# Optimization experiments

Measured on AMD Instinct MI355X. Metric: run time of the kernel, lower is better.

## Reference

```python
import jax, jax.numpy as jnp
import numpy as np

L, I, H = 4, 256, 512          # layers, input_size, hidden_size
SH, LH, GH = 4, 2, 2            # short/long/global heads
NH, HD, FF = SH + LH + GH, H // (SH + LH + GH), 2 * H
S, B = 1024, 8                  # seq (AST nodes), batch
EPS = 1e-5
NEG = -1e9


def _ln(x, g, b):
    m = jnp.mean(x, axis=-1, keepdims=True)
    v = jnp.var(x, axis=-1, keepdims=True)
    return (x - m) * jax.lax.rsqrt(v + EPS) * g + b


def setup_inputs() -> dict:
    key = jax.random.key(0)
    ks = jax.random.split(key, 10)
    w = lambda k, shape: jax.random.normal(k, shape, jnp.float32) * 0.02
    return {
        "nodes": jax.random.normal(ks[0], (S, B, I), jnp.float32),
        "dist": jax.random.randint(ks[1], (B, S, S), 0, 5, jnp.int32),
        "dense_w": w(ks[2], (H, I)), "dense_b": jnp.zeros((H,), jnp.float32),
        "dense_ln_g": jnp.ones((H,), jnp.float32), "dense_ln_b": jnp.zeros((H,), jnp.float32),
        "qkv_w": w(ks[3], (L, 3 * H, H)), "qkv_b": jnp.zeros((L, 3 * H), jnp.float32),
        "out_w": w(ks[4], (L, H, H)), "out_b": jnp.zeros((L, H), jnp.float32),
        "ln1_g": jnp.ones((L, H), jnp.float32), "ln1_b": jnp.zeros((L, H), jnp.float32),
        "ffn_w1": w(ks[5], (L, FF, H)), "ffn_b1": jnp.zeros((L, FF), jnp.float32),
        "ffn_w2": w(ks[6], (L, H, FF)), "ffn_b2": jnp.zeros((L, H), jnp.float32),
        "ln2_g": jnp.ones((L, H), jnp.float32), "ln2_b": jnp.zeros((L, H), jnp.float32),
        "bn_g": jnp.ones((H,), jnp.float32), "bn_b": jnp.zeros((H,), jnp.float32),
    }


def _mask_bias(dist):
    # dist: [B,S,S] int -> additive bias [B,NH,S,S]
    short = (dist == 1)[:, None]                       # [B,1,S,S]
    longm = (dist >= 1)[:, None]
    globm = jnp.broadcast_to((dist[:, 0:1, :] >= 1)[:, None], (dist.shape[0], 1, S, S))
    allowed = jnp.concatenate([
        jnp.broadcast_to(short, (dist.shape[0], SH, S, S)),
        jnp.broadcast_to(longm, (dist.shape[0], LH, S, S)),
        jnp.broadcast_to(globm, (dist.shape[0], GH, S, S)),
    ], axis=1)
    allowed = allowed | jnp.eye(S, dtype=bool)
    return jnp.where(allowed, 0.0, NEG).astype(jnp.float32)


def _forward(nodes, dist, dense_w, dense_b, dense_ln_g, dense_ln_b,
             qkv_w, qkv_b, out_w, out_b, ln1_g, ln1_b,
             ffn_w1, ffn_b1, ffn_w2, ffn_b2, ln2_g, ln2_b, bn_g, bn_b):
    x = jnp.transpose(nodes, (1, 0, 2))                # [B,S,I]
    x = _ln(x @ dense_w.T + dense_b, dense_ln_g, dense_ln_b)  # [B,S,H]
    bias = _mask_bias(dist)                            # [B,NH,S,S]
    scale = 1.0 / np.sqrt(HD)

    def layer(x, p):
        (wqkv, bqkv, wo, bo, g1, b1, w1, bf1, w2, bf2, g2, b2) = p
        qkv = x @ wqkv.T + bqkv                        # [B,S,3H]
        q, k, v = jnp.split(qkv, 3, axis=-1)
        q = q.reshape(B, S, NH, HD).transpose(0, 2, 1, 3)
        k = k.reshape(B, S, NH, HD).transpose(0, 2, 1, 3)
        v = v.reshape(B, S, NH, HD).transpose(0, 2, 1, 3)
        scores = jnp.einsum('bhqd,bhkd->bhqk', q, k) * scale + bias
        attn = jax.nn.softmax(scores, axis=-1)
        o = jnp.einsum('bhqk,bhkd->bhqd', attn, v)
        o = o.transpose(0, 2, 1, 3).reshape(B, S, H) @ wo.T + bo
        x = _ln(x + o, g1, b1)
        f = jax.nn.relu(x @ w1.T + bf1) @ w2.T + bf2
        x = _ln(x + f, g2, b2)
        return x, None

    params = (qkv_w, qkv_b, out_w, out_b, ln1_g, ln1_b,
              ffn_w1, ffn_b1, ffn_w2, ffn_b2, ln2_g, ln2_b)
    x, _ = jax.lax.scan(layer, x, params)
    hidden = x[:, 0]                                   # first token -> [B,H]
    m = jnp.mean(hidden, axis=0)
    v = jnp.var(hidden, axis=0)
    return (hidden - m) * jax.lax.rsqrt(v + EPS) * bn_g + bn_b


def reference(nodes, dist, dense_w, dense_b, dense_ln_g, dense_ln_b,
              qkv_w, qkv_b, out_w, out_b, ln1_g, ln1_b,
              ffn_w1, ffn_b1, ffn_w2, ffn_b2, ln2_g, ln2_b, bn_g, bn_b):
    return _forward(nodes, dist, dense_w, dense_b, dense_ln_g, dense_ln_b,
                    qkv_w, qkv_b, out_w, out_b, ln1_g, ln1_b,
                    ffn_w1, ffn_b1, ffn_w2, ffn_b2, ln2_g, ln2_b, bn_g, bn_b)
```

## Files before the change

kernel.cpp:

```cpp
#include <hip/hip_runtime.h>
#include <hip/hip_bf16.h>
#include <math.h>

#define LAYERS 4
#define IDIM 256
#define HDIM 512
#define NH 8
#define HD 64
#define FF 1024
#define SEQ 1024
#define BATCH 8
#define EPS 1e-5f

typedef __attribute__((ext_vector_type(8))) short short8;
typedef __attribute__((ext_vector_type(4))) short short4v;
typedef __attribute__((ext_vector_type(4))) float f32x4;
typedef __attribute__((ext_vector_type(4))) int int4v;
typedef __attribute__((ext_vector_type(4))) unsigned int uint4v;
typedef unsigned long long u64;

__device__ __forceinline__ short f2bf(float f) {
    unsigned u = __float_as_uint(f);
    u = (u + 0x7FFFu + ((u >> 16) & 1u)) >> 16;
    return (short)u;
}
__device__ __forceinline__ float bf2f(short s) {
    return __uint_as_float(((unsigned)(unsigned short)s) << 16);
}
__device__ __forceinline__ void gll16(const void* g, void* l) {
    __builtin_amdgcn_global_load_lds(
        (const __attribute__((address_space(1))) unsigned int*)g,
        (__attribute__((address_space(3))) unsigned int*)l, 16, 0, 0);
}
__device__ __forceinline__ float fexp2(float x) {
#if __has_builtin(__builtin_amdgcn_exp2f)
    return __builtin_amdgcn_exp2f(x);
#else
    return exp2f(x);
#endif
}

#define CVT_P0 131072u
#define CVT_P1 3276800u
#define CVT_P2 4325376u
#define CVT_P3 6422528u
#define CVT_TOT 8519680u
#define PREP_W 8320
#define PREP_N 2048
__global__ __launch_bounds__(256) void prep_all(
    const float* __restrict__ s0, short* __restrict__ d0,
    const float* __restrict__ s1, short* __restrict__ d1,
    const float* __restrict__ s2, short* __restrict__ d2,
    const float* __restrict__ s3, short* __restrict__ d3,
    const float* __restrict__ s4, short* __restrict__ d4,
    const float* __restrict__ nodes, short* __restrict__ xt,
    const int* __restrict__ dist, u64* __restrict__ mS,
    u64* __restrict__ mL, u64* __restrict__ mG) {
    int blk = blockIdx.x;
    if (blk < PREP_W) {
        size_t i = ((size_t)blk * 256 + threadIdx.x) * 4;
        const float* s; short* d; size_t off;
        if (i < CVT_P0)      { s = s0; d = d0; off = i; }
        else if (i < CVT_P1) { s = s1; d = d1; off = i - CVT_P0; }
        else if (i < CVT_P2) { s = s2; d = d2; off = i - CVT_P1; }
        else if (i < CVT_P3) { s = s3; d = d3; off = i - CVT_P2; }
        else                 { s = s4; d = d4; off = i - CVT_P3; }
        f32x4 f = *(const f32x4*)(s + off);
        short4v o = {f2bf(f[0]), f2bf(f[1]), f2bf(f[2]), f2bf(f[3])};
        *(short4v*)(d + off) = o;
    } else if (blk < PREP_W + PREP_N) {
        size_t idx = ((size_t)(blk - PREP_W) * 256 + threadIdx.x) * 4;
        int i  = idx & (IDIM - 1);
        int sb = idx >> 8;
        int b  = sb & (BATCH - 1);
        int s  = sb >> 3;
        f32x4 f = *(const f32x4*)(nodes + idx);
        short4v o = {f2bf(f[0]), f2bf(f[1]), f2bf(f[2]), f2bf(f[3])};
        *(short4v*)(xt + ((size_t)b * SEQ + s) * IDIM + i) = o;
    } else {
        int blk2 = blk - (PREP_W + PREP_N);
        int b = blk2 >> 10, q = blk2 & 1023;
        int wv = threadIdx.x >> 6, lane = threadIdx.x & 63;
        const int* dp = dist + ((size_t)b * SEQ + q) * SEQ;
        size_t mbase = ((size_t)b * SEQ + q) * 16;
#pragma unroll
        for (int it = 0; it < 4; it++) {
            int w64 = it * 4 + wv;
            int d = dp[w64 * 64 + lane];
            u64 bs = __ballot(d == 1);
            u64 bl = __ballot(d >= 1);
            if (lane == 0) {
                mS[mbase + w64] = bs;
                mL[mbase + w64] = bl;
                if (q == 0) mG[b * 16 + w64] = bl;
            }
        }
    }
}

template<int BM, int BK>
__global__ __launch_bounds__(256, 2)
void gemm_bf16(const short* __restrict__ A, const short* __restrict__ W,
               const float* __restrict__ bias, short* __restrict__ C,
               short* __restrict__ vt, int M, int N, int K, int relu) {
    constexpr int UPR = BK / 8;
    constexpr int RPC = 512 / BK;
    __shared__ __align__(16) short As[BM * BK];
    __shared__ __align__(16) short Ws[128 * BK];
    const int tid = threadIdx.x;
    const int w = tid >> 6, lane = tid & 63;
    const int l15 = lane & 15, quad = lane >> 4;
    const int m0 = blockIdx.y * BM, n0 = blockIdx.x * 128;

    constexpr int NI = (BM == 128) ? 4 : 2;
    const int wm = (BM == 128) ? (w >> 1) * 64 : 0;
    const int wn = (BM == 128) ? (w & 1) * 64 : w * 32;

    f32x4 acc[4][NI];
#pragma unroll
    for (int mi = 0; mi < 4; mi++)
#pragma unroll
        for (int ni = 0; ni < NI; ni++) acc[mi][ni] = (f32x4){0.f, 0.f, 0.f, 0.f};

    const int r_in = (BK == 64) ? (lane >> 3) : (lane >> 4);
    const int c8   = lane & (UPR - 1);

    for (int k0 = 0; k0 < K; k0 += BK) {
#pragma unroll
        for (int rep = 0; rep < BM * BK / 2048; rep++) {
            int chunk = rep * 4 + w;
            int row = chunk * RPC + r_in;
            const short* src = A + (size_t)(m0 + row) * K + k0 + ((c8 ^ (row & (UPR - 1))) << 3);
            gll16(src, (char*)As + chunk * 1024);
        }
#pragma unroll
        for (int rep = 0; rep < 128 * BK / 2048; rep++) {
            int chunk = rep * 4 + w;
            int row = chunk * RPC + r_in;
            const short* src = W + (size_t)(n0 + row) * K + k0 + ((c8 ^ (row & (UPR - 1))) << 3);
            gll16(src, (char*)Ws + chunk * 1024);
        }
        __syncthreads();
#pragma unroll
        for (int ks = 0; ks < BK / 32; ks++) {
            short8 af[4], wf[NI];
            const int dblk = ks * 4 + quad;
#pragma unroll
            for (int mi = 0; mi < 4; mi++) {
                int row = wm + mi * 16 + l15;
                af[mi] = *(const short8*)((const char*)As + row * (BK * 2) + ((dblk ^ (row & (UPR - 1))) << 4));
            }
#pragma unroll
            for (int ni = 0; ni < NI; ni++) {
                int row = wn + ni * 16 + l15;
                wf[ni] = *(const short8*)((const char*)Ws + row * (BK * 2) + ((dblk ^ (row & (UPR - 1))) << 4));
            }
#pragma unroll
            for (int mi = 0; mi < 4; mi++)
#pragma unroll
                for (int ni = 0; ni < NI; ni++)
                    acc[mi][ni] = __builtin_amdgcn_mfma_f32_16x16x32_bf16(
                        af[mi], wf[ni], acc[mi][ni], 0, 0, 0);
        }
        __syncthreads();
    }
    if (vt && n0 >= 1024) {
#pragma unroll
        for (int ni = 0; ni < NI; ni++) {
            int n = n0 + wn + ni * 16 + l15;
            int d = n - 1024, h = d >> 6, dd = d & 63;
            float bz = bias[n];
#pragma unroll
            for (int mi = 0; mi < 4; mi++) {
                int mbase = m0 + wm + mi * 16 + quad * 4;
                int b = mbase >> 10, s = mbase & 1023;
                size_t off = ((size_t)(b * NH + h) * HD + dd) * SEQ + s;
                short4v pk;
#pragma unroll
                for (int r = 0; r < 4; r++) pk[r] = f2bf(acc[mi][ni][r] + bz);
                *(short4v*)(vt + off) = pk;
            }
        }
    } else {
#pragma unroll
        for (int ni = 0; ni < NI; ni++) {
            int n = n0 + wn + ni * 16 + l15;
            float bz = bias[n];
#pragma unroll
            for (int mi = 0; mi < 4; mi++) {
#pragma unroll
                for (int r = 0; r < 4; r++) {
                    int m = m0 + wm + mi * 16 + quad * 4 + r;
                    float v = acc[mi][ni][r] + bz;
                    if (relu) v = fmaxf(v, 0.f);
                    C[(size_t)m * N + n] = f2bf(v);
                }
            }
        }
    }
}

template<int K, bool RES>
__global__ __launch_bounds__(512, 1)
void gemm_ln(const short* __restrict__ A, const short* __restrict__ W,
             const float* __restrict__ bias, const short* __restrict__ resid,
             const float* __restrict__ g, const float* __restrict__ bta,
             short* __restrict__ Y) {
    constexpr int BK = 64, BM = 32, NW = 512, NT = K / BK;
    __shared__ __align__(16) short As[2][BM * BK];
    __shared__ __align__(16) short Ws[2][NW * BK];
    const int tid = threadIdx.x, w = tid >> 6, lane = tid & 63;
    const int l15 = lane & 15, quad = lane >> 4;
    const int m0 = blockIdx.x * BM;
    const int r_in = lane >> 3, c8 = lane & 7;
    const int swz = (c8 ^ r_in) << 3;

    f32x4 acc[2][4];
#pragma unroll
    for (int mi = 0; mi < 2; mi++)
#pragma unroll
        for (int ni = 0; ni < 4; ni++) acc[mi][ni] = (f32x4){0.f, 0.f, 0.f, 0.f};

#define STAGE_LN(bf, k0)                                                          \
    do {                                                                          \
        if (w < 4) {                                                              \
            int row_ = w * 8 + r_in;                                              \
            gll16(A + (size_t)(m0 + row_) * K + (k0) + swz,                       \
                  (char*)As[bf] + w * 1024);                                      \
        }                                                                         \
        _Pragma("unroll")                                                         \
        for (int rep_ = 0; rep_ < 8; rep_++) {                                    \
            int chunk_ = rep_ * 8 + w;                                            \
            int row_ = chunk_ * 8 + r_in;                                         \
            gll16(W + (size_t)row_ * K + (k0) + swz,                              \
                  (char*)Ws[bf] + chunk_ * 1024);                                 \
        }                                                                         \
    } while (0)

    STAGE_LN(0, 0);
    __syncthreads();
    int cur = 0;
    for (int t = 0; t < NT; t++) {
        if (t + 1 < NT) STAGE_LN(cur ^ 1, (t + 1) * BK);
#pragma unroll
        for (int ks = 0; ks < 2; ks++) {
            const int dblk = ks * 4 + quad;
            short8 af[2];
#pragma unroll
            for (int mi = 0; mi < 2; mi++) {
                int row = mi * 16 + l15;
                af[mi] = *(const short8*)((const char*)As[cur] + row * 128 + ((dblk ^ (row & 7)) << 4));
            }
#pragma unroll
            for (int ni = 0; ni < 4; ni++) {
                int row = w * 64 + ni * 16 + l15;
                short8 wf = *(const short8*)((const char*)Ws[cur] + row * 128 + ((dblk ^ (row & 7)) << 4));
#pragma unroll
                for (int mi = 0; mi < 2; mi++)
                    acc[mi][ni] = __builtin_amdgcn_mfma_f32_16x16x32_bf16(
                        wf, af[mi], acc[mi][ni], 0, 0, 0);
            }
        }
        __syncthreads();
        cur ^= 1;
    }
#undef STAGE_LN

    float sum[2] = {0.f, 0.f}, sq[2] = {0.f, 0.f};
#pragma unroll
    for (int mi = 0; mi < 2; mi++)
#pragma unroll
        for (int ni = 0; ni < 4; ni++) {
            int nb = w * 64 + ni * 16 + quad * 4;
            f32x4 bz = *(const f32x4*)(bias + nb);
            f32x4 v;
            if (RES) {
                short4v rv = *(const short4v*)(resid + (size_t)(m0 + mi * 16 + l15) * NW + nb);
#pragma unroll
                for (int r = 0; r < 4; r++) v[r] = acc[mi][ni][r] + bz[r] + bf2f(rv[r]);
            } else {
#pragma unroll
                for (int r = 0; r < 4; r++) v[r] = acc[mi][ni][r] + bz[r];
            }
            acc[mi][ni] = v;
            sum[mi] += v[0] + v[1] + v[2] + v[3];
            sq[mi]  += v[0] * v[0] + v[1] * v[1] + v[2] * v[2] + v[3] * v[3];
        }
#pragma unroll
    for (int mi = 0; mi < 2; mi++) {
        sum[mi] += __shfl_xor(sum[mi], 16); sum[mi] += __shfl_xor(sum[mi], 32);
        sq[mi]  += __shfl_xor(sq[mi], 16);  sq[mi]  += __shfl_xor(sq[mi], 32);
    }
    float* red = (float*)As;
    if (quad == 0) {
#pragma unroll
        for (int mi = 0; mi < 2; mi++) {
            red[(mi * 16 + l15) * 8 + w]       = sum[mi];
            red[256 + (mi * 16 + l15) * 8 + w] = sq[mi];
        }
    }
    __syncthreads();
    float mean[2], inv[2];
#pragma unroll
    for (int mi = 0; mi < 2; mi++) {
        f32x4 s0 = *(const f32x4*)(red + (mi * 16 + l15) * 8);
        f32x4 s1 = *(const f32x4*)(red + (mi * 16 + l15) * 8 + 4);
        f32x4 q0 = *(const f32x4*)(red + 256 + (mi * 16 + l15) * 8);
        f32x4 q1 = *(const f32x4*)(red + 256 + (mi * 16 + l15) * 8 + 4);
        float st = s0[0] + s0[1] + s0[2] + s0[3] + s1[0] + s1[1] + s1[2] + s1[3];
        float qt = q0[0] + q0[1] + q0[2] + q0[3] + q1[0] + q1[1] + q1[2] + q1[3];
        float mn = st * (1.f / NW);
        float vr = qt * (1.f / NW) - mn * mn;
        mean[mi] = mn;
        inv[mi]  = rsqrtf(vr + EPS);
    }
#pragma unroll
    for (int mi = 0; mi < 2; mi++)
#pragma unroll
        for (int ni = 0; ni < 4; ni++) {
            int nb = w * 64 + ni * 16 + quad * 4;
            f32x4 gv = *(const f32x4*)(g + nb);
            f32x4 bv = *(const f32x4*)(bta + nb);
            short4v pk;
#pragma unroll
            for (int r = 0; r < 4; r++)
                pk[r] = f2bf((acc[mi][ni][r] - mean[mi]) * inv[mi] * gv[r] + bv[r]);
            *(short4v*)(Y + (size_t)(m0 + mi * 16 + l15) * NW + nb) = pk;
        }
}

__global__ __launch_bounds__(512, 1)
void fused_ffn(const short* __restrict__ X, const short* __restrict__ W1,
               const float* __restrict__ b1, const short* __restrict__ W2,
               const float* __restrict__ b2, const float* __restrict__ g,
               const float* __restrict__ bta, short* __restrict__ Y) {
    __shared__ __align__(16) char smem[135168];
    short* As1 = (short*)smem;
    char*  W1s = smem + 4096;
    char*  Hs  = smem;
    char*  W2s = smem + 65536;
    float* red = (float*)(smem + 131072);

    const int tid = threadIdx.x, w = tid >> 6, lane = tid & 63;
    const int l15 = lane & 15, quad = lane >> 4;
    const int m0 = blockIdx.x * 32;
    const int r_in = lane >> 3, c8 = lane & 7;
    const int swz = (c8 ^ r_in) << 3;

    f32x4 acc1[2][8];
#pragma unroll
    for (int mi = 0; mi < 2; mi++)
#pragma unroll
        for (int ni = 0; ni < 8; ni++) acc1[mi][ni] = (f32x4){0.f, 0.f, 0.f, 0.f};

    for (int t = 0; t < 8; t++) {
        if (w < 4) {
            int row = w * 8 + r_in;
            gll16(X + (size_t)(m0 + row) * HDIM + t * 64 + swz,
                  (char*)As1 + w * 1024);
        }
#pragma unroll
        for (int rep = 0; rep < 16; rep++) {
            int c = rep * 8 + w;
            int row = c * 8 + r_in;
            gll16(W1 + (size_t)row * HDIM + t * 64 + swz, W1s + c * 1024);
        }
        __syncthreads();
#pragma unroll
        for (int ks = 0; ks < 2; ks++) {
            const int dblk = ks * 4 + quad;
            short8 af[2];
#pragma unroll
            for (int mi = 0; mi < 2; mi++) {
                int row = mi * 16 + l15;
                af[mi] = *(const short8*)((const char*)As1 + row * 128 + ((dblk ^ (row & 7)) << 4));
            }
#pragma unroll
            for (int ni = 0; ni < 8; ni++) {
                int row = w * 128 + ni * 16 + l15;
                short8 wf = *(const short8*)(W1s + row * 128 + ((dblk ^ (row & 7)) << 4));
#pragma unroll
                for (int mi = 0; mi < 2; mi++)
                    acc1[mi][ni] = __builtin_amdgcn_mfma_f32_16x16x32_bf16(
                        wf, af[mi], acc1[mi][ni], 0, 0, 0);
            }
        }
        __syncthreads();
    }

#pragma unroll
    for (int mi = 0; mi < 2; mi++)
#pragma unroll
        for (int ni = 0; ni < 8; ni++) {
            int n = w * 128 + ni * 16 + quad * 4;
            f32x4 bz = *(const f32x4*)(b1 + n);
            short4v pk;
#pragma unroll
            for (int r = 0; r < 4; r++)
                pk[r] = f2bf(fmaxf(acc1[mi][ni][r] + bz[r], 0.f));
            int row = mi * 16 + l15;
            int u = n >> 3;
            *(short4v*)(Hs + row * 2048 + ((u ^ (row & 7)) << 4) + (quad & 1) * 8) = pk;
        }

    f32x4 acc2[2][4];
#pragma unroll
    for (int mi = 0; mi < 2; mi++)
#pragma unroll
        for (int ni = 0; ni < 4; ni++) acc2[mi][ni] = (f32x4){0.f, 0.f, 0.f, 0.f};

    for (int t2 = 0; t2 < 16; t2++) {
#pragma unroll
        for (int rep = 0; rep < 8; rep++) {
            int c = rep * 8 + w;
            int row = c * 8 + r_in;
            gll16(W2 + (size_t)row * FF + t2 * 64 + swz, W2s + c * 1024);
        }
        __syncthreads();
#pragma unroll
        for (int ks = 0; ks < 2; ks++) {
            const int dblk = ks * 4 + quad;
            short8 af[2];
#pragma unroll
            for (int mi = 0; mi < 2; mi++) {
                int row = mi * 16 + l15;
                af[mi] = *(const short8*)(Hs + row * 2048 + (((t2 * 8 + dblk) ^ (row & 7)) << 4));
            }
#pragma unroll
            for (int ni = 0; ni < 4; ni++) {
                int row = w * 64 + ni * 16 + l15;
                short8 wf = *(const short8*)(W2s + row * 128 + ((dblk ^ (row & 7)) << 4));
#pragma unroll
                for (int mi = 0; mi < 2; mi++)
                    acc2[mi][ni] = __builtin_amdgcn_mfma_f32_16x16x32_bf16(
                        wf, af[mi], acc2[mi][ni], 0, 0, 0);
            }
        }
        __syncthreads();
    }

    float sum[2] = {0.f, 0.f}, sq[2] = {0.f, 0.f};
#pragma unroll
    for (int mi = 0; mi < 2; mi++)
#pragma unroll
        for (int ni = 0; ni < 4; ni++) {
            int nb = w * 64 + ni * 16 + quad * 4;
            f32x4 bz = *(const f32x4*)(b2 + nb);
            short4v rv = *(const short4v*)(X + (size_t)(m0 + mi * 16 + l15) * HDIM + nb);
            f32x4 v;
#pragma unroll
            for (int r = 0; r < 4; r++) v[r] = acc2[mi][ni][r] + bz[r] + bf2f(rv[r]);
            acc2[mi][ni] = v;
            sum[mi] += v[0] + v[1] + v[2] + v[3];
            sq[mi]  += v[0] * v[0] + v[1] * v[1] + v[2] * v[2] + v[3] * v[3];
        }
#pragma unroll
    for (int mi = 0; mi < 2; mi++) {
        sum[mi] += __shfl_xor(sum[mi], 16); sum[mi] += __shfl_xor(sum[mi], 32);
        sq[mi]  += __shfl_xor(sq[mi], 16);  sq[mi]  += __shfl_xor(sq[mi], 32);
    }
    if (quad == 0) {
#pragma unroll
        for (int mi = 0; mi < 2; mi++) {
            red[(mi * 16 + l15) * 8 + w]       = sum[mi];
            red[256 + (mi * 16 + l15) * 8 + w] = sq[mi];
        }
    }
    __syncthreads();
    float mean[2], inv[2];
#pragma unroll
    for (int mi = 0; mi < 2; mi++) {
        f32x4 s0 = *(const f32x4*)(red + (mi * 16 + l15) * 8);
        f32x4 s1 = *(const f32x4*)(red + (mi * 16 + l15) * 8 + 4);
        f32x4 q0 = *(const f32x4*)(red + 256 + (mi * 16 + l15) * 8);
        f32x4 q1 = *(const f32x4*)(red + 256 + (mi * 16 + l15) * 8 + 4);
        float st = s0[0] + s0[1] + s0[2] + s0[3] + s1[0] + s1[1] + s1[2] + s1[3];
        float qt = q0[0] + q0[1] + q0[2] + q0[3] + q1[0] + q1[1] + q1[2] + q1[3];
        float mn = st * (1.f / HDIM);
        float vr = qt * (1.f / HDIM) - mn * mn;
        mean[mi] = mn;
        inv[mi]  = rsqrtf(vr + EPS);
    }
#pragma unroll
    for (int mi = 0; mi < 2; mi++)
#pragma unroll
        for (int ni = 0; ni < 4; ni++) {
            int nb = w * 64 + ni * 16 + quad * 4;
            f32x4 gv = *(const f32x4*)(g + nb);
            f32x4 bv = *(const f32x4*)(bta + nb);
            short4v pk;
#pragma unroll
            for (int r = 0; r < 4; r++)
                pk[r] = f2bf((acc2[mi][ni][r] - mean[mi]) * inv[mi] * gv[r] + bv[r]);
            *(short4v*)(Y + (size_t)(m0 + mi * 16 + l15) * HDIM + nb) = pk;
        }
}

#define EXP2SC 0.18033688011112042f
__global__ __launch_bounds__(256, 4)
void attn_mfma(const short* __restrict__ qkv, const short* __restrict__ vt,
               const u64* __restrict__ maskS, const u64* __restrict__ maskL,
               const u64* __restrict__ maskG, short* __restrict__ out) {
    const int tid = threadIdx.x;
    const int w = tid >> 6, lane = tid & 63, l15 = lane & 15, quad = lane >> 4;
    const int p = blockIdx.x;
    const int g_ = (p & 7) + 8 * (p >> 7);
    const int qt = (p >> 3) & 15;
    const int b = g_ >> 3, h = g_ & 7;
    const int q = qt * 64 + w * 16 + l15;

    __shared__ __align__(16) short Ks[128 * 64];
    __shared__ __align__(16) short Vs[128 * 64];

    short8 qf[2];
    {
        const short* qrow = qkv + ((size_t)(b * SEQ + q) * 1536) + h * 64;
#pragma unroll
        for (int ks = 0; ks < 2; ks++)
            qf[ks] = *(const short8*)(qrow + ks * 32 + quad * 8);
    }
    const u64* mrow = (h < 4) ? (maskS + ((size_t)b * SEQ + q) * 16)
                   : (h < 6) ? (maskL + ((size_t)b * SEQ + q) * 16)
                   :           (maskG + (size_t)b * 16);

    f32x4 of[4];
#pragma unroll
    for (int mt = 0; mt < 4; mt++) of[mt] = (f32x4){0.f, 0.f, 0.f, 0.f};
    float ls0 = 0.f, ls1 = 0.f;

    const int r_in = lane >> 3, c8 = lane & 7;
    const int swz = (c8 ^ r_in) << 3;
    const short* kbase = qkv + ((size_t)b * SEQ) * 1536 + 512 + h * 64 + swz;
    const short* vp = vt + ((size_t)((b * NH + h) * HD) + r_in) * SEQ + swz;
    const int fsw = (l15 & 7);

    for (int kt = 0; kt < SEQ; kt += 128) {
#pragma unroll
        for (int rep = 0; rep < 4; rep++) {
            int c = rep * 4 + w;
            int pr = c * 8 + r_in;
            int pt = pr & 63;
            int key = (pr & 64) | (pt & 32) | (((pt >> 2) & 3) << 3)
                    | (((pt >> 4) & 1) << 2) | (pt & 3);
            gll16(kbase + (size_t)(kt + key) * 1536, (char*)Ks + c * 1024);
        }
#pragma unroll
        for (int rep = 0; rep < 4; rep++) {
            int v = rep * 4 + w;
            gll16(vp + (size_t)((v & 7) * 8) * SEQ + kt + (v >> 3) * 64,
                  (char*)Vs + v * 1024);
        }
        __syncthreads();

#pragma unroll
        for (int t = 0; t < 2; t++) {
            f32x4 sa[4];
#pragma unroll
            for (int g = 0; g < 4; g++) sa[g] = (f32x4){0.f, 0.f, 0.f, 0.f};
#pragma unroll
            for (int ks = 0; ks < 2; ks++) {
                const int dblk = ks * 4 + quad;
#pragma unroll
                for (int g = 0; g < 4; g++) {
                    int row = t * 64 + g * 16 + l15;
                    short8 kf = *(const short8*)((const char*)Ks + row * 128 + ((dblk ^ fsw) << 4));
                    sa[g] = __builtin_amdgcn_mfma_f32_16x16x32_bf16(kf, qf[ks], sa[g], 0, 0, 0);
                }
            }
            u64 mw = mrow[(kt >> 6) + t];
            if ((q >> 6) == (kt >> 6) + t) mw |= 1ull << (q & 63);
            u64 mq2 = mw >> (quad * 8);
            unsigned mlo = (unsigned)mq2, mhi = (unsigned)(mq2 >> 32);
            float pv[4][4];
#pragma unroll
            for (int g = 0; g < 4; g++) {
                unsigned mg = ((g & 2) ? mhi : mlo) >> ((g & 1) * 4);
#pragma unroll
                for (int r = 0; r < 4; r++) {
                    float e = fexp2(sa[g][r] * EXP2SC);
                    e = ((mg >> r) & 1u) ? e : 0.f;
                    pv[g][r] = e;
                    if (g & 1) ls1 += e; else ls0 += e;
                }
            }
            short8 pfrag[2];
#pragma unroll
            for (int g32 = 0; g32 < 2; g32++) {
                uint4v pk;
                pk[0] = __builtin_amdgcn_perm(__float_as_uint(pv[2 * g32][1]),
                                              __float_as_uint(pv[2 * g32][0]), 0x07060302u);
                pk[1] = __builtin_amdgcn_perm(__float_as_uint(pv[2 * g32][3]),
                                              __float_as_uint(pv[2 * g32][2]), 0x07060302u);
                pk[2] = __builtin_amdgcn_perm(__float_as_uint(pv[2 * g32 + 1][1]),
                                              __float_as_uint(pv[2 * g32 + 1][0]), 0x07060302u);
                pk[3] = __builtin_amdgcn_perm(__float_as_uint(pv[2 * g32 + 1][3]),
                                              __float_as_uint(pv[2 * g32 + 1][2]), 0x07060302u);
                pfrag[g32] = __builtin_bit_cast(short8, pk);
            }
#pragma unroll
            for (int g32 = 0; g32 < 2; g32++) {
                const int u = g32 * 4 + quad;
#pragma unroll
                for (int mt = 0; mt < 4; mt++) {
                    int row = mt * 16 + l15;
                    short8 vf = *(const short8*)((const char*)Vs + t * 8192 + row * 128 + ((u ^ fsw) << 4));
                    of[mt] = __builtin_amdgcn_mfma_f32_16x16x32_bf16(vf, pfrag[g32], of[mt], 0, 0, 0);
                }
            }
        }
        __syncthreads();
    }
    float lsum = ls0 + ls1;
    lsum += __shfl_xor(lsum, 16);
    lsum += __shfl_xor(lsum, 32);
    float inv = 1.f / lsum;
#pragma unroll
    for (int mt = 0; mt < 4; mt++) {
        short4v pk;
#pragma unroll
        for (int r = 0; r < 4; r++) pk[r] = f2bf(of[mt][r] * inv);
        *(short4v*)(out + ((size_t)(b * SEQ + q) * HDIM) + h * 64 + mt * 16 + quad * 4) = pk;
    }
}

__global__ __launch_bounds__(256) void final_bn(const short* __restrict__ X,
                                                const float* __restrict__ g,
                                                const float* __restrict__ bb,
                                                float* __restrict__ out) {
    int h = blockIdx.x * 256 + threadIdx.x;
    if (h >= HDIM) return;
    float vals[BATCH];
    float m = 0.f;
#pragma unroll
    for (int b = 0; b < BATCH; b++) {
        vals[b] = bf2f(X[(size_t)b * SEQ * HDIM + h]);
        m += vals[b];
    }
    m *= (1.f / BATCH);
    float v = 0.f;
#pragma unroll
    for (int b = 0; b < BATCH; b++) { float d = vals[b] - m; v += d * d; }
    v *= (1.f / BATCH);
    float inv = rsqrtf(v + EPS);
#pragma unroll
    for (int b = 0; b < BATCH; b++)
        out[b * HDIM + h] = (vals[b] - m) * inv * g[h] + bb[h];
}

extern "C" void kernel_launch(void* const* d_in, const int* in_sizes, int n_in,
                              void* d_out, int out_size, void* d_ws, size_t ws_size,
                              hipStream_t stream) {
    const float* nodes      = (const float*)d_in[0];
    const int*   dist       = (const int*)  d_in[1];
    const float* dense_w    = (const float*)d_in[2];
    const float* dense_b    = (const float*)d_in[3];
    const float* dense_ln_g = (const float*)d_in[4];
    const float* dense_ln_b = (const float*)d_in[5];
    const float* qkv_w      = (const float*)d_in[6];
    const float* qkv_b      = (const float*)d_in[7];
    const float* out_w      = (const float*)d_in[8];
    const float* out_b      = (const float*)d_in[9];
    const float* ln1_g      = (const float*)d_in[10];
    const float* ln1_b      = (const float*)d_in[11];
    const float* ffn_w1     = (const float*)d_in[12];
    const float* ffn_b1     = (const float*)d_in[13];
    const float* ffn_w2     = (const float*)d_in[14];
    const float* ffn_b2     = (const float*)d_in[15];
    const float* ln2_g      = (const float*)d_in[16];
    const float* ln2_b      = (const float*)d_in[17];
    const float* bn_g       = (const float*)d_in[18];
    const float* bn_b       = (const float*)d_in[19];
    float* out = (float*)d_out;

    const int M = BATCH * SEQ;
    const size_t MB = 1024 * 1024;
    char* ws = (char*)d_ws;
    short* Wd   = (short*)(ws + 0 * MB);
    short* Wqkv = (short*)(ws + 1 * MB);
    short* Wo   = (short*)(ws + 9 * MB);
    short* W1   = (short*)(ws + 13 * MB);
    short* W2   = (short*)(ws + 18 * MB);
    u64*   mS   = (u64*)(ws + 23 * MB);
    u64*   mL   = (u64*)(ws + 24 * MB);
    u64*   mG   = (u64*)(ws + 25 * MB);
    short* X    = (short*)(ws + 26 * MB);
    short* QKV  = (short*)(ws + 34 * MB);
    short* Vt   = (short*)(ws + 58 * MB);
    short* AT   = (short*)(ws + 66 * MB);
    short* XT   = QKV;

    prep_all<<<PREP_W + PREP_N + BATCH * SEQ, 256, 0, stream>>>(
        dense_w, Wd, qkv_w, Wqkv, out_w, Wo, ffn_w1, W1, ffn_w2, W2,
        nodes, XT, dist, mS, mL, mG);

    gemm_ln<IDIM, false><<<M / 32, 512, 0, stream>>>(
        XT, Wd, dense_b, nullptr, dense_ln_g, dense_ln_b, X);

    for (int l = 0; l < LAYERS; l++) {
        const short* wqkv = Wqkv + (size_t)l * 3 * HDIM * HDIM;
        const float* bqkv = qkv_b + (size_t)l * 3 * HDIM;
        const short* wo   = Wo + (size_t)l * HDIM * HDIM;
        const float* bo   = out_b + (size_t)l * HDIM;
        const short* w1   = W1 + (size_t)l * FF * HDIM;
        const float* b1   = ffn_b1 + (size_t)l * FF;
        const short* w2   = W2 + (size_t)l * HDIM * FF;
        const float* b2   = ffn_b2 + (size_t)l * HDIM;

        gemm_bf16<128, 64><<<dim3(3 * HDIM / 128, M / 128), 256, 0, stream>>>(
            X, wqkv, bqkv, QKV, Vt, M, 3 * HDIM, HDIM, 0);
        attn_mfma<<<1024, 256, 0, stream>>>(QKV, Vt, mS, mL, mG, AT);
        gemm_ln<HDIM, true><<<M / 32, 512, 0, stream>>>(
            AT, wo, bo, X, ln1_g + l * HDIM, ln1_b + l * HDIM, X);
        fused_ffn<<<M / 32, 512, 0, stream>>>(
            X, w1, b1, w2, b2, ln2_g + l * HDIM, ln2_b + l * HDIM, X);
    }
    final_bn<<<(HDIM + 255) / 256, 256, 0, stream>>>(X, bn_g, bn_b, out);
}
```

Measured before the change: 618.4 us.

## Pipeline weight tiles with triple-buffered async loads in gemm_ln and fused_ffn

Both gemm_ln and fused_ffn now load the whole A panel into LDS once. The weight tiles are streamed in small 256-row by 32-k chunks through a three-slot ring buffer, with explicit vmcnt waits and raw barriers so loads stay in flight across iterations. In fused_ffn the first W2 chunks are prefetched while the ReLU hidden tile is written, overlapping the second GEMM's load latency. This targets the exposed global-load latency of the old two-stage and fully serialized loops. The cost is more barriers per k-step, hand-counted waitcnt values that must match the outstanding loads, and larger LDS use.

```diff
diff --git a/kernel.cpp b/kernel.cpp
--- a/kernel.cpp
+++ b/kernel.cpp
@@ -39,6 +39,13 @@
     return exp2f(x);
 #endif
 }
+
+#define BAR() __builtin_amdgcn_s_barrier()
+#define SCHED0() __builtin_amdgcn_sched_barrier(0)
+#define VM4() asm volatile("s_waitcnt vmcnt(4)" ::: "memory")
+#define VM2() asm volatile("s_waitcnt vmcnt(2)" ::: "memory")
+#define VM0() asm volatile("s_waitcnt vmcnt(0)" ::: "memory")
+#define LGKM0() asm volatile("s_waitcnt lgkmcnt(0)" ::: "memory")
 
 #define CVT_P0 131072u
 #define CVT_P1 3276800u
@@ -206,251 +213,108 @@
              const float* __restrict__ bias, const short* __restrict__ resid,
              const float* __restrict__ g, const float* __restrict__ bta,
              short* __restrict__ Y) {
-    constexpr int BK = 64, BM = 32, NW = 512, NT = K / BK;
-    __shared__ __align__(16) short As[2][BM * BK];
-    __shared__ __align__(16) short Ws[2][NW * BK];
+    constexpr int NT = K / 16;
+    constexpr int KCN = K / 32;
+    __shared__ __align__(16) char smem[81920];
+    char* Apan = smem;
+    char* Wb   = smem + 32768;
+    float* red = (float*)smem;
+
     const int tid = threadIdx.x, w = tid >> 6, lane = tid & 63;
     const int l15 = lane & 15, quad = lane >> 4;
-    const int m0 = blockIdx.x * BM;
-    const int r_in = lane >> 3, c8 = lane & 7;
-    const int swz = (c8 ^ r_in) << 3;
+    const int m0 = blockIdx.x * 32;
+    const int r4 = lane >> 2, c4 = lane & 3;
 
     f32x4 acc[2][4];
 #pragma unroll
     for (int mi = 0; mi < 2; mi++)
 #pragma unroll
-        for (int ni = 0; ni < 4; ni++) acc[mi][ni] = (f32x4){0.f, 0.f, 0.f, 0.f};
-
-#define STAGE_LN(bf, k0)                                                          \
-    do {                                                                          \
-        if (w < 4) {                                                              \
-            int row_ = w * 8 + r_in;                                              \
-            gll16(A + (size_t)(m0 + row_) * K + (k0) + swz,                       \
-                  (char*)As[bf] + w * 1024);                                      \
-        }                                                                         \
-        _Pragma("unroll")                                                         \
-        for (int rep_ = 0; rep_ < 8; rep_++) {                                    \
-            int chunk_ = rep_ * 8 + w;                                            \
-            int row_ = chunk_ * 8 + r_in;                                         \
-            gll16(W + (size_t)row_ * K + (k0) + swz,                              \
-                  (char*)Ws[bf] + chunk_ * 1024);                                 \
-        }                                                                         \
+        for (int j = 0; j < 4; j++) acc[mi][j] = (f32x4){0.f, 0.f, 0.f, 0.f};
+
+    if constexpr (K == 512) {
+#pragma unroll
+        for (int j = 0; j < 4; j++) {
+            int row = j * 8 + w;
+            gll16(A + (size_t)(m0 + row) * K + ((lane ^ (row & 7)) << 3),
+                  Apan + row * 1024);
+        }
+    } else {
+#pragma unroll
+        for (int j = 0; j < 2; j++) {
+            int li = j * 8 + w;
+            int row = li * 2 + (lane >> 5);
+            gll16(A + (size_t)(m0 + row) * K + (((lane & 31) ^ (row & 7)) << 3),
+                  Apan + li * 1024);
+        }
+    }
+#define GLN_ISSUE(c, bp_)                                                     \
+    do {                                                                      \
+        int rg_ = (c) & 1, kc_ = (c) >> 1;                                    \
+        _Pragma("unroll")                                                     \
+        for (int j_ = 0; j_ < 2; j_++) {                                      \
+            int li_ = j_ * 8 + w;                                             \
+            int gr_ = rg_ * 256 + li_ * 16 + r4;                              \
+            gll16(W + (size_t)gr_ * K + kc_ * 32 + ((c4 ^ (r4 & 3)) << 3),    \
+                  (bp_) + li_ * 1024);                                        \
+        }                                                                     \
     } while (0)
-
-    STAGE_LN(0, 0);
-    __syncthreads();
+    GLN_ISSUE(0, Wb);
+    GLN_ISSUE(1, Wb + 16384);
+    GLN_ISSUE(2, Wb + 32768);
+    VM4();
+    BAR(); SCHED0();
+
     int cur = 0;
-    for (int t = 0; t < NT; t++) {
-        if (t + 1 < NT) STAGE_LN(cur ^ 1, (t + 1) * BK);
-#pragma unroll
-        for (int ks = 0; ks < 2; ks++) {
-            const int dblk = ks * 4 + quad;
-            short8 af[2];
-#pragma unroll
-            for (int mi = 0; mi < 2; mi++) {
-                int row = mi * 16 + l15;
-                af[mi] = *(const short8*)((const char*)As[cur] + row * 128 + ((dblk ^ (row & 7)) << 4));
-            }
-#pragma unroll
-            for (int ni = 0; ni < 4; ni++) {
-                int row = w * 64 + ni * 16 + l15;
-                short8 wf = *(const short8*)((const char*)Ws[cur] + row * 128 + ((dblk ^ (row & 7)) << 4));
+    for (int kc = 0; kc < KCN; kc++) {
+        short8 af[2];
+#pragma unroll
+        for (int mi = 0; mi < 2; mi++) {
+            int ar = mi * 16 + l15;
+            af[mi] = *(const short8*)(Apan + ar * (K * 2) +
+                                      (((kc * 4 + quad) ^ (ar & 7)) << 4));
+        }
+#pragma unroll
+        for (int rg = 0; rg < 2; rg++) {
+            const char* bp = Wb + cur * 16384;
+#pragma unroll
+            for (int ni = 0; ni < 2; ni++) {
+                int rr = w * 32 + ni * 16 + l15;
+                short8 wf = *(const short8*)(bp + rr * 64 + ((quad ^ (rr & 3)) << 4));
 #pragma unroll
                 for (int mi = 0; mi < 2; mi++)
-                    acc[mi][ni] = __builtin_amdgcn_mfma_f32_16x16x32_bf16(
-                        wf, af[mi], acc[mi][ni], 0, 0, 0);
-            }
-        }
-        __syncthreads();
-        cur ^= 1;
-    }
-#undef STAGE_LN
+                    acc[mi][rg * 2 + ni] = __builtin_amdgcn_mfma_f32_16x16x32_bf16(
+                        wf, af[mi], acc[mi][rg * 2 + ni], 0, 0, 0);
+            }
+            BAR(); SCHED0();
+            {
+                int c = kc * 2 + rg + 3;
+                if (c < NT)           { GLN_ISSUE(c, Wb + cur * 16384); VM4(); }
+                else if (c == NT)     VM2();
+                else if (c == NT + 1) VM0();
+            }
+            BAR(); SCHED0();
+            cur = (cur == 2) ? 0 : cur + 1;
+        }
+    }
+#undef GLN_ISSUE
 
     float sum[2] = {0.f, 0.f}, sq[2] = {0.f, 0.f};
 #pragma unroll
     for (int mi = 0; mi < 2; mi++)
 #pragma unroll
-        for (int ni = 0; ni < 4; ni++) {
-            int nb = w * 64 + ni * 16 + quad * 4;
+        for (int j = 0; j < 4; j++) {
+            int nb = (j >> 1) * 256 + w * 32 + (j & 1) * 16 + quad * 4;
             f32x4 bz = *(const f32x4*)(bias + nb);
             f32x4 v;
             if (RES) {
-                short4v rv = *(const short4v*)(resid + (size_t)(m0 + mi * 16 + l15) * NW + nb);
-#pragma unroll
-                for (int r = 0; r < 4; r++) v[r] = acc[mi][ni][r] + bz[r] + bf2f(rv[r]);
+                short4v rv = *(const short4v*)(resid + (size_t)(m0 + mi * 16 + l15) * HDIM + nb);
+#pragma unroll
+                for (int r = 0; r < 4; r++) v[r] = acc[mi][j][r] + bz[r] + bf2f(rv[r]);
             } else {
 #pragma unroll
-                for (int r = 0; r < 4; r++) v[r] = acc[mi][ni][r] + bz[r];
-            }
-            acc[mi][ni] = v;
-            sum[mi] += v[0] + v[1] + v[2] + v[3];
-            sq[mi]  += v[0] * v[0] + v[1] * v[1] + v[2] * v[2] + v[3] * v[3];
-        }
-#pragma unroll
-    for (int mi = 0; mi < 2; mi++) {
-        sum[mi] += __shfl_xor(sum[mi], 16); sum[mi] += __shfl_xor(sum[mi], 32);
-        sq[mi]  += __shfl_xor(sq[mi], 16);  sq[mi]  += __shfl_xor(sq[mi], 32);
-    }
-    float* red = (float*)As;
-    if (quad == 0) {
-#pragma unroll
-        for (int mi = 0; mi < 2; mi++) {
-            red[(mi * 16 + l15) * 8 + w]       = sum[mi];
-            red[256 + (mi * 16 + l15) * 8 + w] = sq[mi];
-        }
-    }
-    __syncthreads();
-    float mean[2], inv[2];
-#pragma unroll
-    for (int mi = 0; mi < 2; mi++) {
-        f32x4 s0 = *(const f32x4*)(red + (mi * 16 + l15) * 8);
-        f32x4 s1 = *(const f32x4*)(red + (mi * 16 + l15) * 8 + 4);
-        f32x4 q0 = *(const f32x4*)(red + 256 + (mi * 16 + l15) * 8);
-        f32x4 q1 = *(const f32x4*)(red + 256 + (mi * 16 + l15) * 8 + 4);
-        float st = s0[0] + s0[1] + s0[2] + s0[3] + s1[0] + s1[1] + s1[2] + s1[3];
-        float qt = q0[0] + q0[1] + q0[2] + q0[3] + q1[0] + q1[1] + q1[2] + q1[3];
-        float mn = st * (1.f / NW);
-        float vr = qt * (1.f / NW) - mn * mn;
-        mean[mi] = mn;
-        inv[mi]  = rsqrtf(vr + EPS);
-    }
-#pragma unroll
-    for (int mi = 0; mi < 2; mi++)
-#pragma unroll
-        for (int ni = 0; ni < 4; ni++) {
-            int nb = w * 64 + ni * 16 + quad * 4;
-            f32x4 gv = *(const f32x4*)(g + nb);
-            f32x4 bv = *(const f32x4*)(bta + nb);
-            short4v pk;
-#pragma unroll
-            for (int r = 0; r < 4; r++)
-                pk[r] = f2bf((acc[mi][ni][r] - mean[mi]) * inv[mi] * gv[r] + bv[r]);
-            *(short4v*)(Y + (size_t)(m0 + mi * 16 + l15) * NW + nb) = pk;
-        }
-}
-
-__global__ __launch_bounds__(512, 1)
-void fused_ffn(const short* __restrict__ X, const short* __restrict__ W1,
-               const float* __restrict__ b1, const short* __restrict__ W2,
-               const float* __restrict__ b2, const float* __restrict__ g,
-               const float* __restrict__ bta, short* __restrict__ Y) {
-    __shared__ __align__(16) char smem[135168];
-    short* As1 = (short*)smem;
-    char*  W1s = smem + 4096;
-    char*  Hs  = smem;
-    char*  W2s = smem + 65536;
-    float* red = (float*)(smem + 131072);
-
-    const int tid = threadIdx.x, w = tid >> 6, lane = tid & 63;
-    const int l15 = lane & 15, quad = lane >> 4;
-    const int m0 = blockIdx.x * 32;
-    const int r_in = lane >> 3, c8 = lane & 7;
-    const int swz = (c8 ^ r_in) << 3;
-
-    f32x4 acc1[2][8];
-#pragma unroll
-    for (int mi = 0; mi < 2; mi++)
-#pragma unroll
-        for (int ni = 0; ni < 8; ni++) acc1[mi][ni] = (f32x4){0.f, 0.f, 0.f, 0.f};
-
-    for (int t = 0; t < 8; t++) {
-        if (w < 4) {
-            int row = w * 8 + r_in;
-            gll16(X + (size_t)(m0 + row) * HDIM + t * 64 + swz,
-                  (char*)As1 + w * 1024);
-        }
-#pragma unroll
-        for (int rep = 0; rep < 16; rep++) {
-            int c = rep * 8 + w;
-            int row = c * 8 + r_in;
-            gll16(W1 + (size_t)row * HDIM + t * 64 + swz, W1s + c * 1024);
-        }
-        __syncthreads();
-#pragma unroll
-        for (int ks = 0; ks < 2; ks++) {
-            const int dblk = ks * 4 + quad;
-            short8 af[2];
-#pragma unroll
-            for (int mi = 0; mi < 2; mi++) {
-                int row = mi * 16 + l15;
-                af[mi] = *(const short8*)((const char*)As1 + row * 128 + ((dblk ^ (row & 7)) << 4));
-            }
-#pragma unroll
-            for (int ni = 0; ni < 8; ni++) {
-                int row = w * 128 + ni * 16 + l15;
-                short8 wf = *(const short8*)(W1s + row * 128 + ((dblk ^ (row & 7)) << 4));
-#pragma unroll
-                for (int mi = 0; mi < 2; mi++)
-                    acc1[mi][ni] = __builtin_amdgcn_mfma_f32_16x16x32_bf16(
-                        wf, af[mi], acc1[mi][ni], 0, 0, 0);
-            }
-        }
-        __syncthreads();
-    }
-
-#pragma unroll
-    for (int mi = 0; mi < 2; mi++)
-#pragma unroll
-        for (int ni = 0; ni < 8; ni++) {
-            int n = w * 128 + ni * 16 + quad * 4;
-            f32x4 bz = *(const f32x4*)(b1 + n);
-            short4v pk;
-#pragma unroll
-            for (int r = 0; r < 4; r++)
-                pk[r] = f2bf(fmaxf(acc1[mi][ni][r] + bz[r], 0.f));
-            int row = mi * 16 + l15;
-            int u = n >> 3;
-            *(short4v*)(Hs + row * 2048 + ((u ^ (row & 7)) << 4) + (quad & 1) * 8) = pk;
-        }
-
-    f32x4 acc2[2][4];
-#pragma unroll
-    for (int mi = 0; mi < 2; mi++)
-#pragma unroll
-        for (int ni = 0; ni < 4; ni++) acc2[mi][ni] = (f32x4){0.f, 0.f, 0.f, 0.f};
-
-    for (int t2 = 0; t2 < 16; t2++) {
-#pragma unroll
-        for (int rep = 0; rep < 8; rep++) {
-            int c = rep * 8 + w;
-            int row = c * 8 + r_in;
-            gll16(W2 + (size_t)row * FF + t2 * 64 + swz, W2s + c * 1024);
-        }
-        __syncthreads();
-#pragma unroll
-        for (int ks = 0; ks < 2; ks++) {
-            const int dblk = ks * 4 + quad;
-            short8 af[2];
-#pragma unroll
-            for (int mi = 0; mi < 2; mi++) {
-                int row = mi * 16 + l15;
-                af[mi] = *(const short8*)(Hs + row * 2048 + (((t2 * 8 + dblk) ^ (row & 7)) << 4));
-            }
-#pragma unroll
-            for (int ni = 0; ni < 4; ni++) {
-                int row = w * 64 + ni * 16 + l15;
-                short8 wf = *(const short8*)(W2s + row * 128 + ((dblk ^ (row & 7)) << 4));
-#pragma unroll
-                for (int mi = 0; mi < 2; mi++)
-                    acc2[mi][ni] = __builtin_amdgcn_mfma_f32_16x16x32_bf16(
-                        wf, af[mi], acc2[mi][ni], 0, 0, 0);
-            }
-        }
-        __syncthreads();
-    }
-
-    float sum[2] = {0.f, 0.f}, sq[2] = {0.f, 0.f};
-#pragma unroll
-    for (int mi = 0; mi < 2; mi++)
-#pragma unroll
-        for (int ni = 0; ni < 4; ni++) {
-            int nb = w * 64 + ni * 16 + quad * 4;
-            f32x4 bz = *(const f32x4*)(b2 + nb);
-            short4v rv = *(const short4v*)(X + (size_t)(m0 + mi * 16 + l15) * HDIM + nb);
-            f32x4 v;
-#pragma unroll
-            for (int r = 0; r < 4; r++) v[r] = acc2[mi][ni][r] + bz[r] + bf2f(rv[r]);
-            acc2[mi][ni] = v;
+                for (int r = 0; r < 4; r++) v[r] = acc[mi][j][r] + bz[r];
+            }
+            acc[mi][j] = v;
             sum[mi] += v[0] + v[1] + v[2] + v[3];
             sq[mi]  += v[0] * v[0] + v[1] * v[1] + v[2] * v[2] + v[3] * v[3];
         }
@@ -484,14 +348,222 @@
 #pragma unroll
     for (int mi = 0; mi < 2; mi++)
 #pragma unroll
-        for (int ni = 0; ni < 4; ni++) {
-            int nb = w * 64 + ni * 16 + quad * 4;
+        for (int j = 0; j < 4; j++) {
+            int nb = (j >> 1) * 256 + w * 32 + (j & 1) * 16 + quad * 4;
             f32x4 gv = *(const f32x4*)(g + nb);
             f32x4 bv = *(const f32x4*)(bta + nb);
             short4v pk;
 #pragma unroll
             for (int r = 0; r < 4; r++)
-                pk[r] = f2bf((acc2[mi][ni][r] - mean[mi]) * inv[mi] * gv[r] + bv[r]);
+                pk[r] = f2bf((acc[mi][j][r] - mean[mi]) * inv[mi] * gv[r] + bv[r]);
+            *(short4v*)(Y + (size_t)(m0 + mi * 16 + l15) * HDIM + nb) = pk;
+        }
+}
+
+__global__ __launch_bounds__(512, 1)
+void fused_ffn(const short* __restrict__ X, const short* __restrict__ W1,
+               const float* __restrict__ b1, const short* __restrict__ W2,
+               const float* __restrict__ b2, const float* __restrict__ g,
+               const float* __restrict__ bta, short* __restrict__ Y) {
+    __shared__ __align__(16) char smem[147456];
+    char* Apan = smem;
+    char* Wb   = smem + 32768;
+    char* Hs   = smem + 81920;
+    float* red = (float*)smem;
+
+    const int tid = threadIdx.x, w = tid >> 6, lane = tid & 63;
+    const int l15 = lane & 15, quad = lane >> 4;
+    const int m0 = blockIdx.x * 32;
+    const int r4 = lane >> 2, c4 = lane & 3;
+
+    f32x4 acc1[2][8];
+#pragma unroll
+    for (int mi = 0; mi < 2; mi++)
+#pragma unroll
+        for (int j = 0; j < 8; j++) acc1[mi][j] = (f32x4){0.f, 0.f, 0.f, 0.f};
+
+#pragma unroll
+    for (int j = 0; j < 4; j++) {
+        int row = j * 8 + w;
+        gll16(X + (size_t)(m0 + row) * HDIM + ((lane ^ (row & 7)) << 3),
+              Apan + row * 1024);
+    }
+#define FF1_ISSUE(c, bp_)                                                     \
+    do {                                                                      \
+        int rg_ = (c) & 3, kc_ = (c) >> 2;                                    \
+        _Pragma("unroll")                                                     \
+        for (int j_ = 0; j_ < 2; j_++) {                                      \
+            int li_ = j_ * 8 + w;                                             \
+            int gr_ = rg_ * 256 + li_ * 16 + r4;                              \
+            gll16(W1 + (size_t)gr_ * HDIM + kc_ * 32 + ((c4 ^ (r4 & 3)) << 3),\
+                  (bp_) + li_ * 1024);                                        \
+        }                                                                     \
+    } while (0)
+#define FF2_ISSUE(c, bp_)                                                     \
+    do {                                                                      \
+        int rg_ = (c) & 1, kc_ = (c) >> 1;                                    \
+        _Pragma("unroll")                                                     \
+        for (int j_ = 0; j_ < 2; j_++) {                                      \
+            int li_ = j_ * 8 + w;                                             \
+            int gr_ = rg_ * 256 + li_ * 16 + r4;                              \
+            gll16(W2 + (size_t)gr_ * FF + kc_ * 32 + ((c4 ^ (r4 & 3)) << 3),  \
+                  (bp_) + li_ * 1024);                                        \
+        }                                                                     \
+    } while (0)
+    FF1_ISSUE(0, Wb);
+    FF1_ISSUE(1, Wb + 16384);
+    FF1_ISSUE(2, Wb + 32768);
+    VM4();
+    BAR(); SCHED0();
+
+    int cur = 0;
+    for (int kc = 0; kc < 16; kc++) {
+        short8 af[2];
+#pragma unroll
+        for (int mi = 0; mi < 2; mi++) {
+            int ar = mi * 16 + l15;
+            af[mi] = *(const short8*)(Apan + ar * 1024 +
+                                      (((kc * 4 + quad) ^ (ar & 7)) << 4));
+        }
+#pragma unroll
+        for (int rg = 0; rg < 4; rg++) {
+            const char* bp = Wb + cur * 16384;
+#pragma unroll
+            for (int ni = 0; ni < 2; ni++) {
+                int rr = w * 32 + ni * 16 + l15;
+                short8 wf = *(const short8*)(bp + rr * 64 + ((quad ^ (rr & 3)) << 4));
+#pragma unroll
+                for (int mi = 0; mi < 2; mi++)
+                    acc1[mi][rg * 2 + ni] = __builtin_amdgcn_mfma_f32_16x16x32_bf16(
+                        wf, af[mi], acc1[mi][rg * 2 + ni], 0, 0, 0);
+            }
+            BAR(); SCHED0();
+            {
+                int c = kc * 4 + rg + 3;
+                if (c < 64)      { FF1_ISSUE(c, Wb + cur * 16384); VM4(); }
+                else if (c == 64) VM2();
+                else if (c == 65) VM0();
+            }
+            BAR(); SCHED0();
+            cur = (cur == 2) ? 0 : cur + 1;
+        }
+    }
+
+    FF2_ISSUE(0, Wb);
+    FF2_ISSUE(1, Wb + 16384);
+    FF2_ISSUE(2, Wb + 32768);
+#pragma unroll
+    for (int mi = 0; mi < 2; mi++)
+#pragma unroll
+        for (int j = 0; j < 8; j++) {
+            int n = (j >> 1) * 256 + w * 32 + (j & 1) * 16 + quad * 4;
+            f32x4 bz = *(const f32x4*)(b1 + n);
+            short4v pk;
+#pragma unroll
+            for (int r = 0; r < 4; r++)
+                pk[r] = f2bf(fmaxf(acc1[mi][j][r] + bz[r], 0.f));
+            int row = mi * 16 + l15;
+            int u = n >> 3;
+            *(short4v*)(Hs + row * 2048 + ((u ^ (row & 7)) << 4) + (quad & 1) * 8) = pk;
+        }
+    LGKM0();
+    VM4();
+    BAR(); SCHED0();
+
+    f32x4 acc2[2][4];
+#pragma unroll
+    for (int mi = 0; mi < 2; mi++)
+#pragma unroll
+        for (int j = 0; j < 4; j++) acc2[mi][j] = (f32x4){0.f, 0.f, 0.f, 0.f};
+
+    cur = 0;
+    for (int kc = 0; kc < 32; kc++) {
+        short8 af[2];
+#pragma unroll
+        for (int mi = 0; mi < 2; mi++) {
+            int ar = mi * 16 + l15;
+            af[mi] = *(const short8*)(Hs + ar * 2048 +
+                                      (((kc * 4 + quad) ^ (ar & 7)) << 4));
+        }
+#pragma unroll
+        for (int rg = 0; rg < 2; rg++) {
+            const char* bp = Wb + cur * 16384;
+#pragma unroll
+            for (int ni = 0; ni < 2; ni++) {
+                int rr = w * 32 + ni * 16 + l15;
+                short8 wf = *(const short8*)(bp + rr * 64 + ((quad ^ (rr & 3)) << 4));
+#pragma unroll
+                for (int mi = 0; mi < 2; mi++)
+                    acc2[mi][rg * 2 + ni] = __builtin_amdgcn_mfma_f32_16x16x32_bf16(
+                        wf, af[mi], acc2[mi][rg * 2 + ni], 0, 0, 0);
+            }
+            BAR(); SCHED0();
+            {
+                int c = kc * 2 + rg + 3;
+                if (c < 64)      { FF2_ISSUE(c, Wb + cur * 16384); VM4(); }
+                else if (c == 64) VM2();
+                else if (c == 65) VM0();
+            }
+            BAR(); SCHED0();
+            cur = (cur == 2) ? 0 : cur + 1;
+        }
+    }
+#undef FF1_ISSUE
+#undef FF2_ISSUE
+
+    float sum[2] = {0.f, 0.f}, sq[2] = {0.f, 0.f};
+#pragma unroll
+    for (int mi = 0; mi < 2; mi++)
+#pragma unroll
+        for (int j = 0; j < 4; j++) {
+            int nb = (j >> 1) * 256 + w * 32 + (j & 1) * 16 + quad * 4;
+            f32x4 bz = *(const f32x4*)(b2 + nb);
+            short4v rv = *(const short4v*)(X + (size_t)(m0 + mi * 16 + l15) * HDIM + nb);
+            f32x4 v;
+#pragma unroll
+            for (int r = 0; r < 4; r++) v[r] = acc2[mi][j][r] + bz[r] + bf2f(rv[r]);
+            acc2[mi][j] = v;
+            sum[mi] += v[0] + v[1] + v[2] + v[3];
+            sq[mi]  += v[0] * v[0] + v[1] * v[1] + v[2] * v[2] + v[3] * v[3];
+        }
+#pragma unroll
+    for (int mi = 0; mi < 2; mi++) {
+        sum[mi] += __shfl_xor(sum[mi], 16); sum[mi] += __shfl_xor(sum[mi], 32);
+        sq[mi]  += __shfl_xor(sq[mi], 16);  sq[mi]  += __shfl_xor(sq[mi], 32);
+    }
+    if (quad == 0) {
+#pragma unroll
+        for (int mi = 0; mi < 2; mi++) {
+            red[(mi * 16 + l15) * 8 + w]       = sum[mi];
+            red[256 + (mi * 16 + l15) * 8 + w] = sq[mi];
+        }
+    }
+    __syncthreads();
+    float mean[2], inv[2];
+#pragma unroll
+    for (int mi = 0; mi < 2; mi++) {
+        f32x4 s0 = *(const f32x4*)(red + (mi * 16 + l15) * 8);
+        f32x4 s1 = *(const f32x4*)(red + (mi * 16 + l15) * 8 + 4);
+        f32x4 q0 = *(const f32x4*)(red + 256 + (mi * 16 + l15) * 8);
+        f32x4 q1 = *(const f32x4*)(red + 256 + (mi * 16 + l15) * 8 + 4);
+        float st = s0[0] + s0[1] + s0[2] + s0[3] + s1[0] + s1[1] + s1[2] + s1[3];
+        float qt = q0[0] + q0[1] + q0[2] + q0[3] + q1[0] + q1[1] + q1[2] + q1[3];
+        float mn = st * (1.f / HDIM);
+        float vr = qt * (1.f / HDIM) - mn * mn;
+        mean[mi] = mn;
+        inv[mi]  = rsqrtf(vr + EPS);
+    }
+#pragma unroll
+    for (int mi = 0; mi < 2; mi++)
+#pragma unroll
+        for (int j = 0; j < 4; j++) {
+            int nb = (j >> 1) * 256 + w * 32 + (j & 1) * 16 + quad * 4;
+            f32x4 gv = *(const f32x4*)(g + nb);
+            f32x4 bv = *(const f32x4*)(bta + nb);
+            short4v pk;
+#pragma unroll
+            for (int r = 0; r < 4; r++)
+                pk[r] = f2bf((acc2[mi][j][r] - mean[mi]) * inv[mi] * gv[r] + bv[r]);
             *(short4v*)(Y + (size_t)(m0 + mi * 16 + l15) * HDIM + nb) = pk;
         }
 }
```

Result: no change. 615.3 us (-0.5%).
